# Kernel tuning notes

Measured on AMD Instinct MI355X. Metric: run time of the kernel, lower is better.

## Reference

```python
import jax, jax.numpy as jnp
import numpy as np

B, N, HIST, PRED, KHOP, H = 64, 1085, 24, 24, 3, 64
FX, FM = 1, 11
F = FX + FM  # node feature dim fed to gnn (12)
E = 17360


def setup_inputs() -> dict:
    key = jax.random.key(0)
    ks = jax.random.split(key, 13)
    s = 0.1
    return {
        "x_hist": jax.random.normal(ks[0], (B, HIST, N, FX), jnp.float32),
        "enc_misc": jax.random.normal(ks[1], (B, HIST, N, FM), jnp.float32),
        "dec": jax.random.normal(ks[2], (B, PRED, N, FM), jnp.float32),
        "We": jax.random.normal(ks[3], (2 * F, F), jnp.float32) * s,
        "be": jnp.zeros((F,), jnp.float32),
        "Wx": jax.random.normal(ks[4], (KHOP, 2 * F, 3 * H), jnp.float32) * s,
        "Wh": jax.random.normal(ks[5], (KHOP, H, 3 * H), jnp.float32) * s,
        "bx": jnp.zeros((KHOP, 3 * H), jnp.float32),
        "bh": jnp.zeros((KHOP, 3 * H), jnp.float32),
        "fc_w": jax.random.normal(ks[6], (KHOP * H, FX), jnp.float32) * s,
        "fc_b": jnp.zeros((FX,), jnp.float32),
        "src": jax.random.randint(ks[7], (E,), 0, N, jnp.int32),
        "dst": jax.random.randint(ks[8], (E,), 0, N, jnp.int32),
    }


def reference(x_hist, enc_misc, dec, We, be, Wx, Wh, bx, bh, fc_w, fc_b, src, dst):
    features = jnp.concatenate([enc_misc, dec], axis=1)  # (B, HIST+PRED, N, FM)

    def gnn(x):  # x: (B, N, F) -> (B, N, F); edge MLP + scatter-sum + residual
        m = jax.nn.relu(jnp.concatenate([x[:, src], x[:, dst]], -1) @ We + be)  # (B,E,F)
        return x + jnp.zeros_like(x).at[:, dst].add(m)

    def gru(x, h, k):  # x: (B*N, 2F), h: (B*N, H)
        g = x @ Wx[k] + bx[k]
        gh = h @ Wh[k] + bh[k]
        r = jax.nn.sigmoid(g[:, :H] + gh[:, :H])
        z = jax.nn.sigmoid(g[:, H:2 * H] + gh[:, H:2 * H])
        n = jnp.tanh(g[:, 2 * H:] + r * gh[:, 2 * H:])
        return (1.0 - z) * n + z * h

    def run_step(hn, xn):  # xn: (B, N, F)
        xg = xn
        new = list(hn)
        for k in range(KHOP):
            xg = gnn(xg)
            x_gru = jnp.concatenate([xg, xn], -1).reshape(B * N, 2 * F)
            new[k] = gru(x_gru, new[k], k)
        return tuple(new)

    h0 = tuple(jnp.zeros((B * N, H), x_hist.dtype) for _ in range(KHOP))

    def hist_step(hn, inp):
        xp, ft = inp  # (B,N,FX), (B,N,FM)
        return run_step(hn, jnp.concatenate([xp, ft], -1)), None

    hist_xs = (jnp.swapaxes(x_hist[:, :HIST - 1], 0, 1),
               jnp.swapaxes(features[:, 1:HIST], 0, 1))
    hn, _ = jax.lax.scan(hist_step, h0, hist_xs)

    def pred_step(carry, ft):
        hn, x = carry
        hn = run_step(hn, jnp.concatenate([x, ft], -1))
        hn_all = jnp.concatenate([h.reshape(B, N, H) for h in hn], -1)  # (B,N,KHOP*H)
        x_new = hn_all @ fc_w + fc_b  # (B, N, FX)
        return (hn, x_new), x_new

    _, ys = jax.lax.scan(pred_step, (hn, x_hist[:, -1]),
                         jnp.swapaxes(features[:, HIST:], 0, 1))
    return jnp.swapaxes(ys, 0, 1)  # (B, PRED, N, FX)
```

## Files before the change

### kernel.cpp

```cpp
#include <hip/hip_runtime.h>

#define NB 64
#define NNODE 1085
#define HIST 24
#define PRED 24
#define KHOP 3
#define HDIM 64
#define FXD 1
#define FMD 11
#define FD 12
#define NE 17360
#define NROWS (NB*NNODE)
#define CHUNK 136

typedef float v4 __attribute__((ext_vector_type(4)));

__device__ __forceinline__ float sigm(float x){ return 1.0f/(1.0f + __expf(-x)); }
__device__ __forceinline__ float tanh_f(float x){ return 1.0f - 2.0f/(__expf(2.0f*x)+1.0f); }

__global__ void csr_count_k(const int* __restrict__ dst, int* __restrict__ deg)
{
    int e = blockIdx.x*256 + threadIdx.x;
    if (e < NE) atomicAdd(&deg[dst[e]], 1);
}

__global__ __launch_bounds__(1024) void csr_scan_k(const int* __restrict__ deg,
                                                   int* __restrict__ offs, int* __restrict__ curs)
{
    __shared__ int s[2][2048];
    int t = threadIdx.x;
    for (int i=t;i<2048;i+=1024) s[0][i] = (i<NNODE) ? deg[i] : 0;
    __syncthreads();
    int cur = 0;
    for (int d=1; d<2048; d<<=1){
        for (int i=t;i<2048;i+=1024){
            int v = s[cur][i];
            if (i>=d) v += s[cur][i-d];
            s[cur^1][i] = v;
        }
        __syncthreads();
        cur ^= 1;
    }
    for (int i=t;i<=NNODE;i+=1024){
        int v = (i==0) ? 0 : s[cur][i-1];
        offs[i] = v;
        if (i<NNODE) curs[i] = v;
    }
}

__global__ void csr_fill_k(const int* __restrict__ dst, int* __restrict__ curs,
                           int* __restrict__ elist)
{
    int e = blockIdx.x*256 + threadIdx.x;
    if (e < NE){
        int d = dst[e];
        int p = atomicAdd(&curs[d], 1);
        elist[p] = e;
    }
}

__global__ void build_xn_k(const float* __restrict__ xsrc, long xs_bs, long xs_off,
                           const float* __restrict__ feat, long f_bs, long f_off,
                           float* __restrict__ xn)
{
    int row = blockIdx.x*256 + threadIdx.x;
    if (row >= NROWS) return;
    int b = row / NNODE, n = row - b*NNODE;
    float v[12];
    v[0] = xsrc[(long)b*xs_bs + xs_off + n];
    const float* fp = feat + (long)b*f_bs + f_off + (long)n*FMD;
    #pragma unroll
    for (int i=0;i<FMD;i++) v[1+i] = fp[i];
    v4* xp = (v4*)(xn + (long)row*FD);
    #pragma unroll
    for (int q=0;q<3;q++){
        v4 tq; tq[0]=v[4*q]; tq[1]=v[4*q+1]; tq[2]=v[4*q+2]; tq[3]=v[4*q+3];
        xp[q]=tq;
    }
}

__global__ __launch_bounds__(256) void gnn_gather_k(const float* __restrict__ x,
    const float* __restrict__ We, const float* __restrict__ be,
    const int* __restrict__ src, const int* __restrict__ dst,
    const int* __restrict__ elist, const int* __restrict__ offs,
    float* __restrict__ out)
{
    __shared__ __align__(16) float x_s[NNODE*FD];
    __shared__ __align__(16) float acc_s[CHUNK*FD];
    __shared__ __align__(16) float w_s[288];
    __shared__ float be_s[12];
    const int t = threadIdx.x;
    const int b = blockIdx.x >> 3, c = blockIdx.x & 7;
    const int n0 = c*CHUNK, n1 = min(NNODE, n0+CHUNK);

    const v4* xg4 = (const v4*)(x + (long)b*NNODE*FD);
    for (int i=t; i<NNODE*FD/4; i+=256) ((v4*)x_s)[i] = xg4[i];
    for (int i=t; i<288; i+=256) w_s[i]=We[i];
    if (t<12) be_s[t]=be[t];
    for (int i=t; i<(n1-n0)*FD; i+=256) acc_s[i]=0.f;
    __syncthreads();

    const int e_beg = offs[n0], e_end = offs[n1];
    const int total = e_end - e_beg;
    const int L = (total + 255) >> 8;
    const int my_beg = e_beg + t*L;
    const int my_end = min(my_beg + L, e_end);

    float accr[12];
    float part[12];
    int cur = -1;

    for (int idx=my_beg; idx<my_end; ++idx){
        int e = elist[idx];
        int sN = src[e], dN = dst[e];
        if (dN != cur){
            if (cur >= 0){
                float* ab = &acc_s[(cur-n0)*FD];
                #pragma unroll
                for (int f=0;f<12;f++) atomicAdd(&ab[f], accr[f]);
            }
            cur = dN;
            #pragma unroll
            for (int f=0;f<12;f++){ accr[f]=0.f; part[f]=be_s[f]; }
            const v4* xdv = (const v4*)&x_s[dN*FD];
            #pragma unroll
            for (int q=0;q<3;q++){
                v4 cc = xdv[q];
                #pragma unroll
                for (int j=0;j<4;j++){
                    float xv = cc[j];
                    int i = (12 + 4*q + j)*12;
                    v4 w0=*(const v4*)&w_s[i];
                    v4 w1=*(const v4*)&w_s[i+4];
                    v4 w2=*(const v4*)&w_s[i+8];
                    #pragma unroll
                    for (int jj=0;jj<4;jj++){
                        part[jj]   += xv*w0[jj];
                        part[4+jj] += xv*w1[jj];
                        part[8+jj] += xv*w2[jj];
                    }
                }
            }
        }
        float m[12];
        #pragma unroll
        for (int f=0;f<12;f++) m[f]=part[f];
        const v4* xsv = (const v4*)&x_s[sN*FD];
        #pragma unroll
        for (int q=0;q<3;q++){
            v4 a = xsv[q];
            #pragma unroll
            for (int j=0;j<4;j++){
                float xv = a[j];
                int i = (4*q + j)*12;
                v4 w0=*(const v4*)&w_s[i];
                v4 w1=*(const v4*)&w_s[i+4];
                v4 w2=*(const v4*)&w_s[i+8];
                #pragma unroll
                for (int jj=0;jj<4;jj++){
                    m[jj]   += xv*w0[jj];
                    m[4+jj] += xv*w1[jj];
                    m[8+jj] += xv*w2[jj];
                }
            }
        }
        #pragma unroll
        for (int f=0;f<12;f++) accr[f] += fmaxf(m[f], 0.f);
    }
    if (cur >= 0){
        float* ab = &acc_s[(cur-n0)*FD];
        #pragma unroll
        for (int f=0;f<12;f++) atomicAdd(&ab[f], accr[f]);
    }
    __syncthreads();

    const int cnt4 = (n1-n0)*FD/4;
    const v4* xs4 = (const v4*)&x_s[n0*FD];
    const v4* ac4 = (const v4*)acc_s;
    v4* ob4 = (v4*)(out + ((long)b*NNODE + n0)*FD);
    for (int i=t; i<cnt4; i+=256) ob4[i] = xs4[i] + ac4[i];
}

#define KC 44
__global__ __launch_bounds__(256) void gru_k(const float* __restrict__ xg, const float* __restrict__ xn,
    float* __restrict__ h, const float* __restrict__ Wx, const float* __restrict__ Wh,
    const float* __restrict__ bx, const float* __restrict__ bh)
{
    __shared__ __align__(16) float A_s[KC][64];
    __shared__ __align__(16) float W_s[KC][192];
    const int tid = threadIdx.x;
    const int tx = tid & 15, ty = tid >> 4;
    const long row0 = (long)blockIdx.x * 64;

    float acc_r[16], acc_z[16], acc_gn[16], acc_ghn[16];
    #pragma unroll
    for (int i=0;i<16;i++){ acc_r[i]=0.f; acc_z[i]=0.f; acc_gn[i]=0.f; acc_ghn[i]=0.f; }

    for (int i=tid; i<KC*192; i+=256){
        int kk = i/192, c = i - kk*192;
        W_s[kk][c] = (kk<24) ? Wx[kk*192+c] : Wh[(kk-24)*192+c];
    }
    for (int i=tid; i<KC*64; i+=256){
        int kk = i>>6, r = i&63;
        long row = row0 + r;
        float v;
        if (kk<12)      v = xg[row*FD+kk];
        else if (kk<24) v = xn[row*FD+(kk-12)];
        else            v = h[row*HDIM + (kk-24)];
        A_s[kk][r]=v;
    }
    __syncthreads();
    #pragma unroll 4
    for (int kk=0;kk<24;kk++){
        v4 av=*(const v4*)&A_s[kk][ty*4];
        v4 wr=*(const v4*)&W_s[kk][tx*4];
        v4 wz=*(const v4*)&W_s[kk][64+tx*4];
        v4 wn=*(const v4*)&W_s[kk][128+tx*4];
        #pragma unroll
        for (int dr=0;dr<4;dr++)
            #pragma unroll
            for (int dc=0;dc<4;dc++){
                acc_r[dr*4+dc]+=av[dr]*wr[dc];
                acc_z[dr*4+dc]+=av[dr]*wz[dc];
                acc_gn[dr*4+dc]+=av[dr]*wn[dc];
            }
    }
    #pragma unroll 4
    for (int kk=24;kk<44;kk++){
        v4 av=*(const v4*)&A_s[kk][ty*4];
        v4 wr=*(const v4*)&W_s[kk][tx*4];
        v4 wz=*(const v4*)&W_s[kk][64+tx*4];
        v4 wn=*(const v4*)&W_s[kk][128+tx*4];
        #pragma unroll
        for (int dr=0;dr<4;dr++)
            #pragma unroll
            for (int dc=0;dc<4;dc++){
                acc_r[dr*4+dc]+=av[dr]*wr[dc];
                acc_z[dr*4+dc]+=av[dr]*wz[dc];
                acc_ghn[dr*4+dc]+=av[dr]*wn[dc];
            }
    }
    __syncthreads();
    for (int i=tid; i<KC*192; i+=256){
        int kk = i/192, c = i - kk*192;
        W_s[kk][c] = Wh[(20+kk)*192+c];
    }
    for (int i=tid; i<KC*64; i+=256){
        int kk = i>>6, r = i&63;
        A_s[kk][r] = h[(row0+r)*HDIM + 20 + kk];
    }
    __syncthreads();
    #pragma unroll 4
    for (int kk=0;kk<44;kk++){
        v4 av=*(const v4*)&A_s[kk][ty*4];
        v4 wr=*(const v4*)&W_s[kk][tx*4];
        v4 wz=*(const v4*)&W_s[kk][64+tx*4];
        v4 wn=*(const v4*)&W_s[kk][128+tx*4];
        #pragma unroll
        for (int dr=0;dr<4;dr++)
            #pragma unroll
            for (int dc=0;dc<4;dc++){
                acc_r[dr*4+dc]+=av[dr]*wr[dc];
                acc_z[dr*4+dc]+=av[dr]*wz[dc];
                acc_ghn[dr*4+dc]+=av[dr]*wn[dc];
            }
    }

    v4 bxr=*(const v4*)&bx[tx*4],     bhr=*(const v4*)&bh[tx*4];
    v4 bxz=*(const v4*)&bx[64+tx*4],  bhz=*(const v4*)&bh[64+tx*4];
    v4 bxn=*(const v4*)&bx[128+tx*4], bhn=*(const v4*)&bh[128+tx*4];
    #pragma unroll
    for (int dr=0;dr<4;dr++){
        long row = row0 + ty*4 + dr;
        v4 hold = *(const v4*)&h[row*HDIM + tx*4];
        v4 hnew;
        #pragma unroll
        for (int dc=0;dc<4;dc++){
            float rr = sigm(acc_r[dr*4+dc] + bxr[dc] + bhr[dc]);
            float zz = sigm(acc_z[dr*4+dc] + bxz[dc] + bhz[dc]);
            float nn = tanh_f(acc_gn[dr*4+dc] + bxn[dc] + rr*(acc_ghn[dr*4+dc] + bhn[dc]));
            hnew[dc] = (1.0f-zz)*nn + zz*hold[dc];
        }
        *(v4*)&h[row*HDIM + tx*4] = hnew;
    }
}

__global__ void fc_k(const float* __restrict__ h, const float* __restrict__ fc_w,
                     const float* __restrict__ fc_b, float* __restrict__ x_cur,
                     float* __restrict__ out, int p)
{
    int row = blockIdx.x*256+threadIdx.x;
    if (row>=NROWS) return;
    float acc = fc_b[0];
    #pragma unroll
    for (int k=0;k<3;k++){
        const float* hb = h + (long)k*NROWS*HDIM + (long)row*HDIM;
        const float* wb = fc_w + k*HDIM;
        #pragma unroll
        for (int q=0;q<16;q++){
            v4 hv=*(const v4*)&hb[q*4];
            v4 wv=*(const v4*)&wb[q*4];
            acc += hv[0]*wv[0]+hv[1]*wv[1]+hv[2]*wv[2]+hv[3]*wv[3];
        }
    }
    x_cur[row]=acc;
    int b=row/NNODE, n=row-b*NNODE;
    out[((long)b*PRED + p)*NNODE + n] = acc;
}

extern "C" void kernel_launch(void* const* d_in, const int* in_sizes, int n_in,
                              void* d_out, int out_size, void* d_ws, size_t ws_size,
                              hipStream_t stream)
{
    const float* x_hist   = (const float*)d_in[0];
    const float* enc_misc = (const float*)d_in[1];
    const float* dec      = (const float*)d_in[2];
    const float* We       = (const float*)d_in[3];
    const float* be       = (const float*)d_in[4];
    const float* Wx       = (const float*)d_in[5];
    const float* Wh       = (const float*)d_in[6];
    const float* bx       = (const float*)d_in[7];
    const float* bh       = (const float*)d_in[8];
    const float* fc_w     = (const float*)d_in[9];
    const float* fc_b     = (const float*)d_in[10];
    const int*   src      = (const int*)d_in[11];
    const int*   dst      = (const int*)d_in[12];
    float* out = (float*)d_out;

    float* h    = (float*)d_ws;
    float* xn   = h  + (size_t)3*NROWS*HDIM;
    float* xg1  = xn + (size_t)NROWS*FD;
    float* xg2  = xg1 + (size_t)NROWS*FD;
    float* xg3  = xg2 + (size_t)NROWS*FD;
    float* x_cur= xg3 + (size_t)NROWS*FD;
    int*   deg  = (int*)(x_cur + NROWS);
    int*   offs = deg + NNODE;
    int*   curs = offs + NNODE + 1;
    int*   elist= curs + NNODE;

    hipMemsetAsync(h, 0, (size_t)3*NROWS*HDIM*sizeof(float), stream);
    hipMemsetAsync(deg, 0, NNODE*sizeof(int), stream);

    const int gE = (NE+255)/256;
    csr_count_k<<<gE,256,0,stream>>>(dst, deg);
    csr_scan_k<<<1,1024,0,stream>>>(deg, offs, curs);
    csr_fill_k<<<gE,256,0,stream>>>(dst, curs, elist);

    const int gRow  = (NROWS+255)/256;
    const int gGat  = NB*8;
    const int gGru  = NROWS/64;

    auto step = [&](const float* xsrc, long xs_bs, long xs_off,
                    const float* feat, long f_bs, long f_off){
        build_xn_k<<<gRow,256,0,stream>>>(xsrc,xs_bs,xs_off,feat,f_bs,f_off,xn);
        gnn_gather_k<<<gGat,256,0,stream>>>(xn, We,be,src,dst,elist,offs, xg1);
        gru_k<<<gGru,256,0,stream>>>(xg1,xn,h,                     Wx,          Wh,          bx,      bh);
        gnn_gather_k<<<gGat,256,0,stream>>>(xg1,We,be,src,dst,elist,offs, xg2);
        gru_k<<<gGru,256,0,stream>>>(xg2,xn,h+(size_t)NROWS*HDIM,  Wx+24*192,   Wh+64*192,   bx+192,  bh+192);
        gnn_gather_k<<<gGat,256,0,stream>>>(xg2,We,be,src,dst,elist,offs, xg3);
        gru_k<<<gGru,256,0,stream>>>(xg3,xn,h+(size_t)2*NROWS*HDIM,Wx+2*24*192, Wh+2*64*192, bx+2*192,bh+2*192);
    };

    for (int t=0;t<HIST-1;t++)
        step(x_hist,(long)HIST*NNODE,(long)t*NNODE,
             enc_misc,(long)HIST*NNODE*FMD,(long)(t+1)*NNODE*FMD);

    for (int p=0;p<PRED;p++){
        if (p==0)
            step(x_hist,(long)HIST*NNODE,(long)(HIST-1)*NNODE,
                 dec,(long)PRED*NNODE*FMD,(long)p*NNODE*FMD);
        else
            step(x_cur,(long)NNODE,0L,
                 dec,(long)PRED*NNODE*FMD,(long)p*NNODE*FMD);
        fc_k<<<gRow,256,0,stream>>>(h, fc_w, fc_b, x_cur, out, p);
    }
}
```

Baseline: 14.42 ms.

## Batch history-step GNN passes across timesteps and fuse three GRU hops per launch

In the history phase the GNN input does not depend on the hidden state, so the three gather passes are run once for a chunk of timesteps using a 2D grid. The chunk size is picked from the available workspace. A new gru3_k handles all three hops in one launch via blockIdx.y, and its shared-memory tile loads are vectorized with v4. This cuts the number of launches and raises parallelism per launch. In exchange it uses a much larger workspace and adds chunk-size logic that depends on ws_size.

```diff
diff --git a/kernel.cpp b/kernel.cpp
--- a/kernel.cpp
+++ b/kernel.cpp
@@ -59,6 +59,27 @@
     }
 }
 
+__global__ void build_hist_k(const float* __restrict__ x_hist, const float* __restrict__ enc_misc,
+                             int t0, int T, float* __restrict__ xn_all)
+{
+    int idx = blockIdx.x*256 + threadIdx.x;
+    if (idx >= T*NROWS) return;
+    int ti = idx / NROWS, row = idx - ti*NROWS;
+    int b = row / NNODE, n = row - b*NNODE;
+    int t = t0 + ti;
+    float v[12];
+    v[0] = x_hist[((long)b*HIST + t)*NNODE + n];
+    const float* fp = enc_misc + (((long)b*HIST + (t+1))*NNODE + n)*FMD;
+    #pragma unroll
+    for (int i=0;i<FMD;i++) v[1+i] = fp[i];
+    v4* xp = (v4*)(xn_all + ((long)ti*NROWS + row)*FD);
+    #pragma unroll
+    for (int q=0;q<3;q++){
+        v4 tq; tq[0]=v[4*q]; tq[1]=v[4*q+1]; tq[2]=v[4*q+2]; tq[3]=v[4*q+3];
+        xp[q]=tq;
+    }
+}
+
 __global__ void build_xn_k(const float* __restrict__ xsrc, long xs_bs, long xs_off,
                            const float* __restrict__ feat, long f_bs, long f_off,
                            float* __restrict__ xn)
@@ -79,11 +100,11 @@
     }
 }
 
-__global__ __launch_bounds__(256) void gnn_gather_k(const float* __restrict__ x,
+__global__ __launch_bounds__(256) void gnn_gather_k(const float* __restrict__ xin,
     const float* __restrict__ We, const float* __restrict__ be,
     const int* __restrict__ src, const int* __restrict__ dst,
     const int* __restrict__ elist, const int* __restrict__ offs,
-    float* __restrict__ out)
+    float* __restrict__ xout)
 {
     __shared__ __align__(16) float x_s[NNODE*FD];
     __shared__ __align__(16) float acc_s[CHUNK*FD];
@@ -91,7 +112,9 @@
     __shared__ float be_s[12];
     const int t = threadIdx.x;
     const int b = blockIdx.x >> 3, c = blockIdx.x & 7;
+    const long ti = blockIdx.y;
     const int n0 = c*CHUNK, n1 = min(NNODE, n0+CHUNK);
+    const float* x = xin + ti*NROWS*FD;
 
     const v4* xg4 = (const v4*)(x + (long)b*NNODE*FD);
     for (int i=t; i<NNODE*FD/4; i+=256) ((v4*)x_s)[i] = xg4[i];
@@ -177,37 +200,64 @@
     const int cnt4 = (n1-n0)*FD/4;
     const v4* xs4 = (const v4*)&x_s[n0*FD];
     const v4* ac4 = (const v4*)acc_s;
-    v4* ob4 = (v4*)(out + ((long)b*NNODE + n0)*FD);
+    v4* ob4 = (v4*)(xout + ti*NROWS*FD + ((long)b*NNODE + n0)*FD);
     for (int i=t; i<cnt4; i+=256) ob4[i] = xs4[i] + ac4[i];
 }
 
 #define KC 44
-__global__ __launch_bounds__(256) void gru_k(const float* __restrict__ xg, const float* __restrict__ xn,
-    float* __restrict__ h, const float* __restrict__ Wx, const float* __restrict__ Wh,
+__global__ __launch_bounds__(256) void gru3_k(
+    const float* __restrict__ xg_base, long k_stride,
+    const float* __restrict__ xn,
+    float* __restrict__ h_base,
+    const float* __restrict__ Wx, const float* __restrict__ Wh,
     const float* __restrict__ bx, const float* __restrict__ bh)
 {
+    const int k = blockIdx.y;
+    const float* xg  = xg_base + (long)k*k_stride;
+    float*       h   = h_base + (size_t)k*NROWS*HDIM;
+    const float* wx  = Wx + (size_t)k*24*192;
+    const float* wh  = Wh + (size_t)k*64*192;
+    const float* bxk = bx + k*192;
+    const float* bhk = bh + k*192;
+
     __shared__ __align__(16) float A_s[KC][64];
     __shared__ __align__(16) float W_s[KC][192];
     const int tid = threadIdx.x;
     const int tx = tid & 15, ty = tid >> 4;
     const long row0 = (long)blockIdx.x * 64;
 
+    const v4* xg4 = (const v4*)(xg + row0*FD);
+    const v4* xn4 = (const v4*)(xn + row0*FD);
+    const v4* h4  = (const v4*)(h  + row0*HDIM);
+    const v4* wx4 = (const v4*)wx;
+    const v4* wh4 = (const v4*)wh;
+
     float acc_r[16], acc_z[16], acc_gn[16], acc_ghn[16];
     #pragma unroll
     for (int i=0;i<16;i++){ acc_r[i]=0.f; acc_z[i]=0.f; acc_gn[i]=0.f; acc_ghn[i]=0.f; }
 
-    for (int i=tid; i<KC*192; i+=256){
-        int kk = i/192, c = i - kk*192;
-        W_s[kk][c] = (kk<24) ? Wx[kk*192+c] : Wh[(kk-24)*192+c];
-    }
-    for (int i=tid; i<KC*64; i+=256){
-        int kk = i>>6, r = i&63;
-        long row = row0 + r;
-        float v;
-        if (kk<12)      v = xg[row*FD+kk];
-        else if (kk<24) v = xn[row*FD+(kk-12)];
-        else            v = h[row*HDIM + (kk-24)];
-        A_s[kk][r]=v;
+    for (int i=tid; i<KC*48; i+=256){
+        int kk = i/48, q = i - kk*48;
+        v4 w = (kk<24) ? wx4[kk*48+q] : wh4[(kk-24)*48+q];
+        *(v4*)&W_s[kk][q*4] = w;
+    }
+    for (int i=tid; i<192; i+=256){
+        int r = i/3, q = i - r*3;
+        v4 v = xg4[r*3+q];
+        #pragma unroll
+        for (int j=0;j<4;j++) A_s[4*q+j][r] = v[j];
+    }
+    for (int i=tid; i<192; i+=256){
+        int r = i/3, q = i - r*3;
+        v4 v = xn4[r*3+q];
+        #pragma unroll
+        for (int j=0;j<4;j++) A_s[12+4*q+j][r] = v[j];
+    }
+    for (int i=tid; i<320; i+=256){
+        int r = i/5, q = i - r*5;
+        v4 v = h4[r*16+q];
+        #pragma unroll
+        for (int j=0;j<4;j++) A_s[24+4*q+j][r] = v[j];
     }
     __syncthreads();
     #pragma unroll 4
@@ -241,13 +291,15 @@
             }
     }
     __syncthreads();
-    for (int i=tid; i<KC*192; i+=256){
-        int kk = i/192, c = i - kk*192;
-        W_s[kk][c] = Wh[(20+kk)*192+c];
-    }
-    for (int i=tid; i<KC*64; i+=256){
-        int kk = i>>6, r = i&63;
-        A_s[kk][r] = h[(row0+r)*HDIM + 20 + kk];
+    for (int i=tid; i<KC*48; i+=256){
+        int kk = i/48, q = i - kk*48;
+        *(v4*)&W_s[kk][q*4] = wh4[(20+kk)*48+q];
+    }
+    for (int i=tid; i<704; i+=256){
+        int r = i/11, q = i - r*11;
+        v4 v = h4[r*16+5+q];
+        #pragma unroll
+        for (int j=0;j<4;j++) A_s[4*q+j][r] = v[j];
     }
     __syncthreads();
     #pragma unroll 4
@@ -266,9 +318,9 @@
             }
     }
 
-    v4 bxr=*(const v4*)&bx[tx*4],     bhr=*(const v4*)&bh[tx*4];
-    v4 bxz=*(const v4*)&bx[64+tx*4],  bhz=*(const v4*)&bh[64+tx*4];
-    v4 bxn=*(const v4*)&bx[128+tx*4], bhn=*(const v4*)&bh[128+tx*4];
+    v4 bxr=*(const v4*)&bxk[tx*4],     bhr=*(const v4*)&bhk[tx*4];
+    v4 bxz=*(const v4*)&bxk[64+tx*4],  bhz=*(const v4*)&bhk[64+tx*4];
+    v4 bxn=*(const v4*)&bxk[128+tx*4], bhn=*(const v4*)&bhk[128+tx*4];
     #pragma unroll
     for (int dr=0;dr<4;dr++){
         long row = row0 + ty*4 + dr;
@@ -327,16 +379,26 @@
     const int*   dst      = (const int*)d_in[12];
     float* out = (float*)d_out;
 
-    float* h    = (float*)d_ws;
-    float* xn   = h  + (size_t)3*NROWS*HDIM;
-    float* xg1  = xn + (size_t)NROWS*FD;
-    float* xg2  = xg1 + (size_t)NROWS*FD;
-    float* xg3  = xg2 + (size_t)NROWS*FD;
-    float* x_cur= xg3 + (size_t)NROWS*FD;
-    int*   deg  = (int*)(x_cur + NROWS);
-    int*   offs = deg + NNODE;
-    int*   curs = offs + NNODE + 1;
-    int*   elist= curs + NNODE;
+    const size_t SZ_T = (size_t)NROWS*FD;
+    size_t fixed_f = (size_t)3*NROWS*HDIM + NROWS + 32*1024;
+    size_t avail_f = ws_size/4;
+    long tc = 1;
+    if (avail_f > fixed_f + 4*SZ_T)
+        tc = (long)((avail_f - fixed_f) / (4*SZ_T));
+    if (tc > HIST-1) tc = HIST-1;
+    if (tc < 1) tc = 1;
+    const long T_CHUNK = tc;
+
+    float* h      = (float*)d_ws;
+    float* x_cur  = h + (size_t)3*NROWS*HDIM;
+    int*   deg    = (int*)(x_cur + NROWS);
+    int*   offs   = deg + NNODE;
+    int*   curs   = offs + NNODE + 1;
+    int*   elist  = curs + NNODE;
+    float* xn_all = (float*)(elist + NE) + 16;
+    xn_all = (float*)(((size_t)xn_all + 63) & ~(size_t)63);
+    float* xg_all = xn_all + T_CHUNK*SZ_T;
+    const long K_STRIDE = T_CHUNK*SZ_T;
 
     hipMemsetAsync(h, 0, (size_t)3*NROWS*HDIM*sizeof(float), stream);
     hipMemsetAsync(deg, 0, NNODE*sizeof(int), stream);
@@ -346,32 +408,35 @@
     csr_scan_k<<<1,1024,0,stream>>>(deg, offs, curs);
     csr_fill_k<<<gE,256,0,stream>>>(dst, curs, elist);
 
-    const int gRow  = (NROWS+255)/256;
-    const int gGat  = NB*8;
-    const int gGru  = NROWS/64;
-
-    auto step = [&](const float* xsrc, long xs_bs, long xs_off,
-                    const float* feat, long f_bs, long f_off){
-        build_xn_k<<<gRow,256,0,stream>>>(xsrc,xs_bs,xs_off,feat,f_bs,f_off,xn);
-        gnn_gather_k<<<gGat,256,0,stream>>>(xn, We,be,src,dst,elist,offs, xg1);
-        gru_k<<<gGru,256,0,stream>>>(xg1,xn,h,                     Wx,          Wh,          bx,      bh);
-        gnn_gather_k<<<gGat,256,0,stream>>>(xg1,We,be,src,dst,elist,offs, xg2);
-        gru_k<<<gGru,256,0,stream>>>(xg2,xn,h+(size_t)NROWS*HDIM,  Wx+24*192,   Wh+64*192,   bx+192,  bh+192);
-        gnn_gather_k<<<gGat,256,0,stream>>>(xg2,We,be,src,dst,elist,offs, xg3);
-        gru_k<<<gGru,256,0,stream>>>(xg3,xn,h+(size_t)2*NROWS*HDIM,Wx+2*24*192, Wh+2*64*192, bx+2*192,bh+2*192);
-    };
-
-    for (int t=0;t<HIST-1;t++)
-        step(x_hist,(long)HIST*NNODE,(long)t*NNODE,
-             enc_misc,(long)HIST*NNODE*FMD,(long)(t+1)*NNODE*FMD);
+    const int gRow = (NROWS+255)/256;
+
+    for (int t0 = 0; t0 < HIST-1; t0 += (int)T_CHUNK){
+        int T = min((int)T_CHUNK, HIST-1-t0);
+        build_hist_k<<<(T*NROWS+255)/256,256,0,stream>>>(x_hist, enc_misc, t0, T, xn_all);
+        dim3 gG(NB*8, T);
+        gnn_gather_k<<<gG,256,0,stream>>>(xn_all,            We,be,src,dst,elist,offs, xg_all);
+        gnn_gather_k<<<gG,256,0,stream>>>(xg_all,            We,be,src,dst,elist,offs, xg_all+K_STRIDE);
+        gnn_gather_k<<<gG,256,0,stream>>>(xg_all+K_STRIDE,   We,be,src,dst,elist,offs, xg_all+2*K_STRIDE);
+        for (int ti=0; ti<T; ti++){
+            dim3 gU(NROWS/64, 3);
+            gru3_k<<<gU,256,0,stream>>>(xg_all + ti*SZ_T, K_STRIDE,
+                                        xn_all + ti*SZ_T, h, Wx, Wh, bx, bh);
+        }
+    }
 
     for (int p=0;p<PRED;p++){
         if (p==0)
-            step(x_hist,(long)HIST*NNODE,(long)(HIST-1)*NNODE,
-                 dec,(long)PRED*NNODE*FMD,(long)p*NNODE*FMD);
+            build_xn_k<<<gRow,256,0,stream>>>(x_hist,(long)HIST*NNODE,(long)(HIST-1)*NNODE,
+                                              dec,(long)PRED*NNODE*FMD,(long)p*NNODE*FMD, xn_all);
         else
-            step(x_cur,(long)NNODE,0L,
-                 dec,(long)PRED*NNODE*FMD,(long)p*NNODE*FMD);
+            build_xn_k<<<gRow,256,0,stream>>>(x_cur,(long)NNODE,0L,
+                                              dec,(long)PRED*NNODE*FMD,(long)p*NNODE*FMD, xn_all);
+        dim3 gG(NB*8, 1);
+        gnn_gather_k<<<gG,256,0,stream>>>(xn_all,          We,be,src,dst,elist,offs, xg_all);
+        gnn_gather_k<<<gG,256,0,stream>>>(xg_all,          We,be,src,dst,elist,offs, xg_all+K_STRIDE);
+        gnn_gather_k<<<gG,256,0,stream>>>(xg_all+K_STRIDE, We,be,src,dst,elist,offs, xg_all+2*K_STRIDE);
+        dim3 gU(NROWS/64, 3);
+        gru3_k<<<gU,256,0,stream>>>(xg_all, K_STRIDE, xn_all, h, Wx, Wh, bx, bh);
         fc_k<<<gRow,256,0,stream>>>(h, fc_w, fc_b, x_cur, out, p);
     }
 }
```

Result: faster. 12.02 ms (-16.7%).
